# Performance work log

Hardware: AMD Instinct MI355X
Metric: run time of the kernel (lower is better)

Reference implementation:

```python
import jax, jax.numpy as jnp
import numpy as np

N = 256      # N' = N (pair rep crop size)
CZ = 128     # c_z
H = 4        # num_heads
DH = 32      # c_hidden per head
INF = 1e9
EPS = 1e-5

def setup_inputs() -> dict:
    key = jax.random.key(0)
    ks = jax.random.split(key, 8)
    s = 0.02
    return {
        "x": jax.random.normal(ks[0], (N, N, CZ), jnp.float32),
        "mask": jnp.ones((N, N), jnp.float32),
        "ln_g": jnp.ones((CZ,), jnp.float32),
        "ln_b": jnp.zeros((CZ,), jnp.float32),
        "w_tri": jax.random.normal(ks[1], (H, CZ), jnp.float32) * s,   # Linear(c_z -> H), no bias
        "wq": jax.random.normal(ks[2], (H * DH, CZ), jnp.float32) * s,
        "wk": jax.random.normal(ks[3], (H * DH, CZ), jnp.float32) * s,
        "wv": jax.random.normal(ks[4], (H * DH, CZ), jnp.float32) * s,
        "wg": jax.random.normal(ks[5], (H * DH, CZ), jnp.float32) * s,
        "bg": jnp.ones((H * DH,), jnp.float32),   # gating bias init = 1 (OpenFold)
        "wo": jax.random.normal(ks[6], (CZ, H * DH), jnp.float32) * s,
        "bo": jnp.zeros((CZ,), jnp.float32),
    }

def reference(x, mask, ln_g, ln_b, w_tri, wq, wk, wv, wg, bg, wo, bo):
    # starting=True -> no transpose. LayerNorm over c_z.
    mu = jnp.mean(x, axis=-1, keepdims=True)
    var = jnp.var(x, axis=-1, keepdims=True)
    xn = (x - mu) * jax.lax.rsqrt(var + EPS) * ln_g + ln_b        # [N', N, CZ]

    # mask bias: [*, N', 1, 1, N]
    mask_bias = (INF * (mask - 1.0))[..., :, None, None, :]
    # triangle bias: linear -> [N', N, H] -> permute (2,0,1) -> [H, N', N] -> [1, H, N', N]
    tri_bias = jnp.einsum('...ijc,hc->...hij', xn, w_tri)[..., None, :, :, :]

    scale = 1.0 / np.sqrt(DH).astype(np.float32)
    wq3, wk3, wv3, wg3 = (w.reshape(H, DH, CZ) for w in (wq, wk, wv, wg))
    q = jnp.einsum('...qc,hdc->...qhd', xn, wq3) * scale           # [N', N, H, DH]
    k = jnp.einsum('...kc,hdc->...khd', xn, wk3)
    v = jnp.einsum('...kc,hdc->...khd', xn, wv3)

    logits = jnp.einsum('...qhd,...khd->...hqk', q, k) + mask_bias + tri_bias  # [N', H, N, N]
    a = jax.nn.softmax(logits, axis=-1)
    o = jnp.einsum('...hqk,...khd->...qhd', a, v)                  # [N', N, H, DH]

    g = jax.nn.sigmoid(jnp.einsum('...qc,hdc->...qhd', xn, wg3) + bg.reshape(H, DH))
    o = (o * g).reshape(*o.shape[:-2], H * DH)                     # [N', N, H*DH]
    return jnp.einsum('...qe,oe->...qo', o, wo) + bo               # [N', N, CZ]
```

## Files before the change

kernel.cpp:

```cpp
#include <hip/hip_runtime.h>
#include <hip/hip_bf16.h>
#include <math.h>


#define NN 256
#define CZ 128
#define NH 4
#define DH 32
#define NPOS (NN * NN)
#define PSZ ((size_t)NPOS * CZ)
#define SCALE 0.17677669529663687f

typedef unsigned short ushort_t;
using f32x4  = __attribute__((ext_vector_type(4))) float;
using bf16x8 = __attribute__((ext_vector_type(8))) short;
using bf16x4 = __attribute__((ext_vector_type(4))) short;

__device__ __forceinline__ float sigmoidf_(float x) {
    return 1.0f / (1.0f + __expf(-x));
}
__device__ __forceinline__ ushort_t f2bf(float f) {
    unsigned u = __float_as_uint(f);
    u = (u + 0x7fffu + ((u >> 16) & 1u)) >> 16;
    return (ushort_t)u;
}
__device__ __forceinline__ float bf2f(ushort_t b) {
    return __uint_as_float(((unsigned)b) << 16);
}
__device__ __forceinline__ float trunc_bf(float f) {
    return __uint_as_float(__float_as_uint(f) & 0xffff0000u);
}
__device__ __forceinline__ bf16x4 pack_bf4(float a, float b, float c, float d) {
    union { unsigned u[2]; bf16x4 v; } r;
    r.u[0] = (__float_as_uint(b) & 0xffff0000u) | (__float_as_uint(a) >> 16);
    r.u[1] = (__float_as_uint(d) & 0xffff0000u) | (__float_as_uint(c) >> 16);
    return r.v;
}

__global__ __launch_bounds__(256)
void convert_weights(const float* __restrict__ wq, const float* __restrict__ wk,
                     const float* __restrict__ wv, const float* __restrict__ wg,
                     const float* __restrict__ wo,
                     ushort_t* __restrict__ Wc_hi, ushort_t* __restrict__ Wc_lo,
                     ushort_t* __restrict__ wo_hi, ushort_t* __restrict__ wo_lo) {
    int idx = blockIdx.x * 256 + threadIdx.x;
    float x;
    if (idx < 65536) {
        int t = idx >> 14;
        const float* src = (t == 0) ? wq : (t == 1) ? wk : (t == 2) ? wv : wg;
        x = src[idx & 16383];
        ushort_t h = f2bf(x);
        Wc_hi[idx] = h;
        Wc_lo[idx] = f2bf(x - bf2f(h));
    } else {
        int r = idx - 65536;
        x = wo[r];
        ushort_t h = f2bf(x);
        wo_hi[r] = h;
        wo_lo[r] = f2bf(x - bf2f(h));
    }
}

__global__ __launch_bounds__(256)
void ln_tri_kernel(const float* __restrict__ x,
                   const float* __restrict__ ln_g,
                   const float* __restrict__ ln_b,
                   const float* __restrict__ w_tri,
                   ushort_t* __restrict__ xn_hi,
                   ushort_t* __restrict__ xn_lo,
                   float* __restrict__ tri) {
    int wave = threadIdx.x >> 6;
    int lane = threadIdx.x & 63;
    int p = blockIdx.x * 4 + wave;
    const float* xp = x + (size_t)p * CZ + lane * 2;
    float2 v = *(const float2*)xp;

    float s = v.x + v.y;
    float sq = v.x * v.x + v.y * v.y;
    #pragma unroll
    for (int off = 1; off < 64; off <<= 1) {
        s  += __shfl_xor(s,  off);
        sq += __shfl_xor(sq, off);
    }
    float mu = s * (1.0f / 128.0f);
    float var = sq * (1.0f / 128.0f) - mu * mu;
    float rs = rsqrtf(var + 1e-5f);

    float2 gv = *(const float2*)(ln_g + lane * 2);
    float2 bv = *(const float2*)(ln_b + lane * 2);
    float xn0 = (v.x - mu) * rs * gv.x + bv.x;
    float xn1 = (v.y - mu) * rs * gv.y + bv.y;

    ushort_t h0 = f2bf(xn0), h1 = f2bf(xn1);
    ushort_t l0 = f2bf(xn0 - bf2f(h0)), l1 = f2bf(xn1 - bf2f(h1));
    ushort2 hh; hh.x = h0; hh.y = h1;
    ushort2 ll; ll.x = l0; ll.y = l1;
    *(ushort2*)(xn_hi + (size_t)p * CZ + lane * 2) = hh;
    *(ushort2*)(xn_lo + (size_t)p * CZ + lane * 2) = ll;

    float t0, t1, t2, t3;
    {
        float2 w0 = *(const float2*)(w_tri + 0 * CZ + lane * 2);
        float2 w1 = *(const float2*)(w_tri + 1 * CZ + lane * 2);
        float2 w2 = *(const float2*)(w_tri + 2 * CZ + lane * 2);
        float2 w3 = *(const float2*)(w_tri + 3 * CZ + lane * 2);
        t0 = xn0 * w0.x + xn1 * w0.y;
        t1 = xn0 * w1.x + xn1 * w1.y;
        t2 = xn0 * w2.x + xn1 * w2.y;
        t3 = xn0 * w3.x + xn1 * w3.y;
    }
    #pragma unroll
    for (int off = 1; off < 64; off <<= 1) {
        t0 += __shfl_xor(t0, off);
        t1 += __shfl_xor(t1, off);
        t2 += __shfl_xor(t2, off);
        t3 += __shfl_xor(t3, off);
    }
    if (lane == 0) {
        int i = p >> 8, j = p & 255;
        int kt = j >> 6, mt = (j >> 4) & 3, kg2 = (j >> 2) & 3, r = j & 3;
        int wv2 = i >> 6, nt = (i >> 4) & 3, lr2 = i & 15;
        size_t base = ((((size_t)(kt * 16 + mt * 4 + wv2)) * 4 + nt) * 64 +
                       kg2 * 16 + lr2) * 4 + r;
        tri[base + 0 * 65536] = t0;
        tri[base + 1 * 65536] = t1;
        tri[base + 2 * 65536] = t2;
        tri[base + 3 * 65536] = t3;
    }
}

template<int MODE>
__global__ __launch_bounds__(256, 2)
void gemm_split_kernel(const ushort_t* __restrict__ Ahi, const ushort_t* __restrict__ Alo,
                       const ushort_t* __restrict__ Bhi, const ushort_t* __restrict__ Blo,
                       float* __restrict__ out0, const float* __restrict__ bias,
                       ushort_t* __restrict__ qbo, ushort_t* __restrict__ kbo,
                       ushort_t* __restrict__ vto, float* __restrict__ gfo) {
    __shared__ ushort_t sA[2][128 * 64];
    __shared__ ushort_t sB[2][128 * 64];

    const int tid = threadIdx.x;
    const int bm = blockIdx.x;
    const int nb0 = blockIdx.y * 128;
    const int lane = tid & 63;
    const int wv_ = tid >> 6;
    const int wm = wv_ >> 1, wn = wv_ & 1;
    const int lr = lane & 15, kg = lane >> 4;

    f32x4 acc[4][4];
    #pragma unroll
    for (int a = 0; a < 4; a++)
        #pragma unroll
        for (int b = 0; b < 4; b++) acc[a][b] = (f32x4){0.f, 0.f, 0.f, 0.f};

    for (int k0 = 0; k0 < CZ; k0 += 64) {
        #pragma unroll
        for (int i = 0; i < 4; i++) {
            int idx = tid + i * 256;
            int row = idx >> 3, c = idx & 7;
            int lofs = row * 64 + ((c ^ (row & 7)) << 3);
            size_t ga = (size_t)(bm * 128 + row) * CZ + k0 + c * 8;
            size_t gb = (size_t)(nb0 + row) * CZ + k0 + c * 8;
            *(uint4*)&sA[0][lofs] = *(const uint4*)(Ahi + ga);
            *(uint4*)&sA[1][lofs] = *(const uint4*)(Alo + ga);
            *(uint4*)&sB[0][lofs] = *(const uint4*)(Bhi + gb);
            *(uint4*)&sB[1][lofs] = *(const uint4*)(Blo + gb);
        }
        __syncthreads();

        #pragma unroll
        for (int ks = 0; ks < 2; ks++) {
            bf16x8 ahi[4], alo[4];
            #pragma unroll
            for (int mt = 0; mt < 4; mt++) {
                int m = wm * 64 + mt * 16 + lr;
                int off = m * 64 + (((ks * 4 + kg) ^ (m & 7)) << 3);
                ahi[mt] = *(bf16x8*)&sA[0][off];
                alo[mt] = *(bf16x8*)&sA[1][off];
            }
            #pragma unroll
            for (int nt = 0; nt < 4; nt++) {
                int n = wn * 64 + nt * 16 + lr;
                int off = n * 64 + (((ks * 4 + kg) ^ (n & 7)) << 3);
                bf16x8 bhi = *(bf16x8*)&sB[0][off];
                bf16x8 blo = *(bf16x8*)&sB[1][off];
                #pragma unroll
                for (int mt = 0; mt < 4; mt++) {
                    acc[mt][nt] = __builtin_amdgcn_mfma_f32_16x16x32_bf16(ahi[mt], bhi, acc[mt][nt], 0, 0, 0);
                    acc[mt][nt] = __builtin_amdgcn_mfma_f32_16x16x32_bf16(alo[mt], bhi, acc[mt][nt], 0, 0, 0);
                    acc[mt][nt] = __builtin_amdgcn_mfma_f32_16x16x32_bf16(ahi[mt], blo, acc[mt][nt], 0, 0, 0);
                }
            }
        }
        __syncthreads();
    }

    #pragma unroll
    for (int mt = 0; mt < 4; mt++) {
        #pragma unroll
        for (int nt = 0; nt < 4; nt++) {
            int n = wn * 64 + nt * 16 + lr;
            #pragma unroll
            for (int r = 0; r < 4; r++) {
                int m = bm * 128 + wm * 64 + mt * 16 + kg * 4 + r;
                float val = acc[mt][nt][r];
                if (MODE == 0) {
                    int t = blockIdx.y;
                    int ii = m >> 8, j = m & 255;
                    int hh = n >> 5, d = n & 31;
                    size_t ihb = (size_t)((ii << 2) + hh) * 8192;
                    if (t == 0)      qbo[ihb + j * 32 + d] = f2bf(val * SCALE);
                    else if (t == 1) kbo[ihb + j * 32 + d] = f2bf(val);
                    else if (t == 2) vto[ihb + d * 256 + j] = f2bf(val);
                    else             gfo[ihb + j * 32 + d] = val;
                } else {
                    out0[(size_t)m * CZ + n] = val + bias[n];
                }
            }
        }
    }
}

__global__ __launch_bounds__(256, 4)
void attn_mfma_kernel(const ushort_t* __restrict__ qb,
                      const ushort_t* __restrict__ kb,
                      const ushort_t* __restrict__ vtb,
                      const float* __restrict__ gf,
                      const float* __restrict__ tri,
                      const float* __restrict__ mask,
                      const float* __restrict__ bg,
                      ushort_t* __restrict__ og_hi,
                      ushort_t* __restrict__ og_lo) {
    __shared__ ushort_t sV[32 * 264];

    const int bid = blockIdx.x;
    const int h = bid >> 8;
    const int i = bid & 255;
    const int tid = threadIdx.x;
    const int lane = tid & 63;
    const int wv_ = tid >> 6;
    const int lr = lane & 15;
    const int kg = lane >> 4;
    const int q0 = wv_ * 64;

    const size_t ih = (size_t)((i << 2) + h);
    const ushort_t* qp = qb + ih * 8192;
    const ushort_t* kp = kb + ih * 8192;
    const ushort_t* vp = vtb + ih * 8192;
    const float* mrow = mask + (i << 8);

    #pragma unroll
    for (int w = 0; w < 4; w++) {
        int idx = tid + w * 256;
        int d = idx >> 5, c = idx & 31;
        *(uint4*)&sV[d * 264 + c * 8] = *(const uint4*)(vp + d * 256 + c * 8);
    }

    bf16x8 qf[4];
    #pragma unroll
    for (int nt = 0; nt < 4; nt++)
        qf[nt] = *(const bf16x8*)(qp + (size_t)(q0 + nt * 16 + lr) * 32 + kg * 8);

    float tl[4] = {0.f, 0.f, 0.f, 0.f};
    f32x4 o[4][2];
    #pragma unroll
    for (int nt = 0; nt < 4; nt++) {
        o[nt][0] = (f32x4){0.f, 0.f, 0.f, 0.f};
        o[nt][1] = (f32x4){0.f, 0.f, 0.f, 0.f};
    }
    __syncthreads();

    for (int kt = 0; kt < 4; kt++) {
        const int kt0 = kt * 64;
        #pragma unroll
        for (int mt = 0; mt < 4; mt++) {
            bf16x8 ka = *(const bf16x8*)(kp + (size_t)(kt0 + mt * 16 + lr) * 32 + kg * 8);
            const float* trib = tri + ((size_t)h << 16) +
                                ((((size_t)(kt * 16 + mt * 4 + wv_)) * 4) * 64 +
                                 kg * 16 + lr) * 4;
            float4 trif[4];
            #pragma unroll
            for (int nt = 0; nt < 4; nt++)
                trif[nt] = *(const float4*)(trib + (size_t)nt * 256);
            float4 mq = *(const float4*)(mrow + kt0 + mt * 16 + kg * 4);
            float mb[4] = {(mq.x - 1.f) * 1e9f, (mq.y - 1.f) * 1e9f,
                           (mq.z - 1.f) * 1e9f, (mq.w - 1.f) * 1e9f};

            f32x4 st[4];
            #pragma unroll
            for (int nt = 0; nt < 4; nt++)
                st[nt] = __builtin_amdgcn_mfma_f32_16x16x32_bf16(
                    ka, qf[nt], (f32x4){0.f, 0.f, 0.f, 0.f}, 0, 0, 0);

            bf16x4 pa[4];
            #pragma unroll
            for (int nt = 0; nt < 4; nt++) {
                float p0 = trunc_bf(__expf(st[nt][0] + mb[0] + trif[nt].x));
                float p1 = trunc_bf(__expf(st[nt][1] + mb[1] + trif[nt].y));
                float p2 = trunc_bf(__expf(st[nt][2] + mb[2] + trif[nt].z));
                float p3 = trunc_bf(__expf(st[nt][3] + mb[3] + trif[nt].w));
                tl[nt] += (p0 + p1) + (p2 + p3);
                pa[nt] = pack_bf4(p0, p1, p2, p3);
            }
            #pragma unroll
            for (int dt = 0; dt < 2; dt++) {
                bf16x4 vb = *(const bf16x4*)&sV[(dt * 16 + lr) * 264 + kt0 + mt * 16 + kg * 4];
                #pragma unroll
                for (int nt = 0; nt < 4; nt++)
                    o[nt][dt] = __builtin_amdgcn_mfma_f32_16x16x16bf16_1k(pa[nt], vb, o[nt][dt], 0, 0, 0);
            }
        }
    }

    #pragma unroll
    for (int nt = 0; nt < 4; nt++) {
        float t = tl[nt];
        t += __shfl_xor(t, 16);
        t += __shfl_xor(t, 32);
        float inv = 1.0f / t;
        #pragma unroll
        for (int r = 0; r < 4; r++) {
            float iv = __shfl(inv, kg * 4 + r, 16);
            int q = q0 + nt * 16 + kg * 4 + r;
            #pragma unroll
            for (int dt = 0; dt < 2; dt++) {
                int d = dt * 16 + lr;
                float gate = sigmoidf_(gf[ih * 8192 + q * 32 + d] + bg[(h << 5) + d]);
                float val = o[nt][dt][r] * iv * gate;
                ushort_t vh = f2bf(val);
                ushort_t vl = f2bf(val - bf2f(vh));
                size_t ofs = (size_t)((i << 8) + q) * CZ + (h << 5) + d;
                og_hi[ofs] = vh;
                og_lo[ofs] = vl;
            }
        }
    }
}

extern "C" void kernel_launch(void* const* d_in, const int* in_sizes, int n_in,
                              void* d_out, int out_size, void* d_ws, size_t ws_size,
                              hipStream_t stream) {
    const float* x     = (const float*)d_in[0];
    const float* mask  = (const float*)d_in[1];
    const float* ln_g  = (const float*)d_in[2];
    const float* ln_b  = (const float*)d_in[3];
    const float* w_tri = (const float*)d_in[4];
    const float* wq    = (const float*)d_in[5];
    const float* wk    = (const float*)d_in[6];
    const float* wv    = (const float*)d_in[7];
    const float* wg    = (const float*)d_in[8];
    const float* bg    = (const float*)d_in[9];
    const float* wo    = (const float*)d_in[10];
    const float* bo    = (const float*)d_in[11];
    float* out = (float*)d_out;

    float* ws = (float*)d_ws;
    float* tri = ws;
    float* gf  = ws + 262144;
    ushort_t* og_hi = (ushort_t*)(gf + PSZ);
    ushort_t* og_lo = og_hi + PSZ;
    ushort_t* qbuf  = og_lo + PSZ;
    ushort_t* kbuf  = qbuf + PSZ;
    ushort_t* vtbuf = kbuf + PSZ;
    ushort_t* Wc_hi = vtbuf + PSZ;
    ushort_t* Wc_lo = Wc_hi + 65536;
    ushort_t* wo_hi = Wc_lo + 65536;
    ushort_t* wo_lo = wo_hi + 16384;
    ushort_t* xn_hi = (ushort_t*)d_out;
    ushort_t* xn_lo = xn_hi + PSZ;

    convert_weights<<<320, 256, 0, stream>>>(wq, wk, wv, wg, wo, Wc_hi, Wc_lo, wo_hi, wo_lo);
    ln_tri_kernel<<<NPOS / 4, 256, 0, stream>>>(x, ln_g, ln_b, w_tri, xn_hi, xn_lo, tri);
    gemm_split_kernel<0><<<dim3(NPOS / 128, 4), 256, 0, stream>>>(
        xn_hi, xn_lo, Wc_hi, Wc_lo, nullptr, nullptr, qbuf, kbuf, vtbuf, gf);
    attn_mfma_kernel<<<NN * NH, 256, 0, stream>>>(
        qbuf, kbuf, vtbuf, gf, tri, mask, bg, og_hi, og_lo);
    gemm_split_kernel<1><<<dim3(NPOS / 128, 1), 256, 0, stream>>>(
        og_hi, og_lo, wo_hi, wo_lo, out, bo, nullptr, nullptr, nullptr, nullptr);
}
```

Before: 259.2 us.

## Load GEMM operands directly into registers and vectorize epilogue stores

Replaces the LDS-staged split-bf16 GEMM with a kernel that loads MFMA operand fragments straight from global memory into registers. This removes the shared-memory round trip and the barriers. The MFMA operands are swapped (W as A) for the q/k/g and output paths so each lane holds four contiguous output columns, which allows 4-wide packed bf16 or float4 stores instead of scalar scattered stores. The V-transpose path keeps the original orientation so it can write 4 contiguous j values. The trade-off is that each wave now does redundant global/L2 loads, since tiles are no longer shared across waves through LDS.

```diff
diff --git a/kernel.cpp b/kernel.cpp
--- a/kernel.cpp
+++ b/kernel.cpp
@@ -34,6 +34,11 @@
     union { unsigned u[2]; bf16x4 v; } r;
     r.u[0] = (__float_as_uint(b) & 0xffff0000u) | (__float_as_uint(a) >> 16);
     r.u[1] = (__float_as_uint(d) & 0xffff0000u) | (__float_as_uint(c) >> 16);
+    return r.v;
+}
+__device__ __forceinline__ bf16x4 pack_bf4_rne(float a, float b, float c, float d) {
+    union { ushort_t s[4]; bf16x4 v; } r;
+    r.s[0] = f2bf(a); r.s[1] = f2bf(b); r.s[2] = f2bf(c); r.s[3] = f2bf(d);
     return r.v;
 }
 
@@ -130,91 +135,117 @@
 }
 
 template<int MODE>
-__global__ __launch_bounds__(256, 2)
-void gemm_split_kernel(const ushort_t* __restrict__ Ahi, const ushort_t* __restrict__ Alo,
-                       const ushort_t* __restrict__ Bhi, const ushort_t* __restrict__ Blo,
-                       float* __restrict__ out0, const float* __restrict__ bias,
-                       ushort_t* __restrict__ qbo, ushort_t* __restrict__ kbo,
-                       ushort_t* __restrict__ vto, float* __restrict__ gfo) {
-    __shared__ ushort_t sA[2][128 * 64];
-    __shared__ ushort_t sB[2][128 * 64];
-
+__global__ __launch_bounds__(256)
+void gemm_direct_kernel(const ushort_t* __restrict__ Xhi, const ushort_t* __restrict__ Xlo,
+                        const ushort_t* __restrict__ Whi, const ushort_t* __restrict__ Wlo,
+                        float* __restrict__ out0, const float* __restrict__ bias,
+                        ushort_t* __restrict__ qbo, ushort_t* __restrict__ kbo,
+                        ushort_t* __restrict__ vto, float* __restrict__ gfo) {
     const int tid = threadIdx.x;
     const int bm = blockIdx.x;
-    const int nb0 = blockIdx.y * 128;
+    const int t = (MODE == 0) ? blockIdx.y : 0;
     const int lane = tid & 63;
     const int wv_ = tid >> 6;
     const int wm = wv_ >> 1, wn = wv_ & 1;
     const int lr = lane & 15, kg = lane >> 4;
 
+    const ushort_t* xh_base = Xhi + ((size_t)(bm * 128 + wm * 64 + lr)) * CZ + kg * 8;
+    const ushort_t* xl_base = Xlo + ((size_t)(bm * 128 + wm * 64 + lr)) * CZ + kg * 8;
+    const ushort_t* wh_base = Whi + ((size_t)(t * 128 + wn * 64 + lr)) * CZ + kg * 8;
+    const ushort_t* wl_base = Wlo + ((size_t)(t * 128 + wn * 64 + lr)) * CZ + kg * 8;
+
     f32x4 acc[4][4];
     #pragma unroll
     for (int a = 0; a < 4; a++)
         #pragma unroll
         for (int b = 0; b < 4; b++) acc[a][b] = (f32x4){0.f, 0.f, 0.f, 0.f};
 
-    for (int k0 = 0; k0 < CZ; k0 += 64) {
-        #pragma unroll
-        for (int i = 0; i < 4; i++) {
-            int idx = tid + i * 256;
-            int row = idx >> 3, c = idx & 7;
-            int lofs = row * 64 + ((c ^ (row & 7)) << 3);
-            size_t ga = (size_t)(bm * 128 + row) * CZ + k0 + c * 8;
-            size_t gb = (size_t)(nb0 + row) * CZ + k0 + c * 8;
-            *(uint4*)&sA[0][lofs] = *(const uint4*)(Ahi + ga);
-            *(uint4*)&sA[1][lofs] = *(const uint4*)(Alo + ga);
-            *(uint4*)&sB[0][lofs] = *(const uint4*)(Bhi + gb);
-            *(uint4*)&sB[1][lofs] = *(const uint4*)(Blo + gb);
-        }
-        __syncthreads();
-
-        #pragma unroll
-        for (int ks = 0; ks < 2; ks++) {
-            bf16x8 ahi[4], alo[4];
-            #pragma unroll
-            for (int mt = 0; mt < 4; mt++) {
-                int m = wm * 64 + mt * 16 + lr;
-                int off = m * 64 + (((ks * 4 + kg) ^ (m & 7)) << 3);
-                ahi[mt] = *(bf16x8*)&sA[0][off];
-                alo[mt] = *(bf16x8*)&sA[1][off];
-            }
+    #pragma unroll
+    for (int ks = 0; ks < 4; ks++) {
+        bf16x8 xh[4], xl[4], wh[4], wl[4];
+        #pragma unroll
+        for (int mt = 0; mt < 4; mt++) {
+            xh[mt] = *(const bf16x8*)(xh_base + (size_t)mt * 16 * CZ + ks * 32);
+            xl[mt] = *(const bf16x8*)(xl_base + (size_t)mt * 16 * CZ + ks * 32);
+        }
+        #pragma unroll
+        for (int nt = 0; nt < 4; nt++) {
+            wh[nt] = *(const bf16x8*)(wh_base + (size_t)nt * 16 * CZ + ks * 32);
+            wl[nt] = *(const bf16x8*)(wl_base + (size_t)nt * 16 * CZ + ks * 32);
+        }
+        if (MODE == 0 && t == 2) {
+            #pragma unroll
+            for (int mt = 0; mt < 4; mt++)
+                #pragma unroll
+                for (int nt = 0; nt < 4; nt++) {
+                    acc[mt][nt] = __builtin_amdgcn_mfma_f32_16x16x32_bf16(xh[mt], wh[nt], acc[mt][nt], 0, 0, 0);
+                    acc[mt][nt] = __builtin_amdgcn_mfma_f32_16x16x32_bf16(xl[mt], wh[nt], acc[mt][nt], 0, 0, 0);
+                    acc[mt][nt] = __builtin_amdgcn_mfma_f32_16x16x32_bf16(xh[mt], wl[nt], acc[mt][nt], 0, 0, 0);
+                }
+        } else {
+            #pragma unroll
+            for (int nt = 0; nt < 4; nt++)
+                #pragma unroll
+                for (int mt = 0; mt < 4; mt++) {
+                    acc[nt][mt] = __builtin_amdgcn_mfma_f32_16x16x32_bf16(wh[nt], xh[mt], acc[nt][mt], 0, 0, 0);
+                    acc[nt][mt] = __builtin_amdgcn_mfma_f32_16x16x32_bf16(wl[nt], xh[mt], acc[nt][mt], 0, 0, 0);
+                    acc[nt][mt] = __builtin_amdgcn_mfma_f32_16x16x32_bf16(wh[nt], xl[mt], acc[nt][mt], 0, 0, 0);
+                }
+        }
+    }
+
+    if (MODE == 1) {
+        #pragma unroll
+        for (int mt = 0; mt < 4; mt++) {
+            int m = bm * 128 + wm * 64 + mt * 16 + lr;
+            #pragma unroll
+            for (int nt = 0; nt < 4; nt++) {
+                int nb = wn * 64 + nt * 16 + kg * 4;
+                float4 bv = *(const float4*)(bias + nb);
+                float4 o;
+                o.x = acc[nt][mt][0] + bv.x;
+                o.y = acc[nt][mt][1] + bv.y;
+                o.z = acc[nt][mt][2] + bv.z;
+                o.w = acc[nt][mt][3] + bv.w;
+                *(float4*)(out0 + (size_t)m * CZ + nb) = o;
+            }
+        }
+    } else if (t == 2) {
+        #pragma unroll
+        for (int mt = 0; mt < 4; mt++) {
+            int m = bm * 128 + wm * 64 + mt * 16 + kg * 4;
+            int i_ = m >> 8, jb = m & 255;
             #pragma unroll
             for (int nt = 0; nt < 4; nt++) {
                 int n = wn * 64 + nt * 16 + lr;
-                int off = n * 64 + (((ks * 4 + kg) ^ (n & 7)) << 3);
-                bf16x8 bhi = *(bf16x8*)&sB[0][off];
-                bf16x8 blo = *(bf16x8*)&sB[1][off];
-                #pragma unroll
-                for (int mt = 0; mt < 4; mt++) {
-                    acc[mt][nt] = __builtin_amdgcn_mfma_f32_16x16x32_bf16(ahi[mt], bhi, acc[mt][nt], 0, 0, 0);
-                    acc[mt][nt] = __builtin_amdgcn_mfma_f32_16x16x32_bf16(alo[mt], bhi, acc[mt][nt], 0, 0, 0);
-                    acc[mt][nt] = __builtin_amdgcn_mfma_f32_16x16x32_bf16(ahi[mt], blo, acc[mt][nt], 0, 0, 0);
-                }
-            }
-        }
-        __syncthreads();
-    }
-
-    #pragma unroll
-    for (int mt = 0; mt < 4; mt++) {
-        #pragma unroll
-        for (int nt = 0; nt < 4; nt++) {
-            int n = wn * 64 + nt * 16 + lr;
-            #pragma unroll
-            for (int r = 0; r < 4; r++) {
-                int m = bm * 128 + wm * 64 + mt * 16 + kg * 4 + r;
-                float val = acc[mt][nt][r];
-                if (MODE == 0) {
-                    int t = blockIdx.y;
-                    int ii = m >> 8, j = m & 255;
-                    int hh = n >> 5, d = n & 31;
-                    size_t ihb = (size_t)((ii << 2) + hh) * 8192;
-                    if (t == 0)      qbo[ihb + j * 32 + d] = f2bf(val * SCALE);
-                    else if (t == 1) kbo[ihb + j * 32 + d] = f2bf(val);
-                    else if (t == 2) vto[ihb + d * 256 + j] = f2bf(val);
-                    else             gfo[ihb + j * 32 + d] = val;
+                int h_ = n >> 5, d = n & 31;
+                size_t ihb = (size_t)((i_ << 2) + h_) * 8192;
+                *(bf16x4*)(vto + ihb + (size_t)d * 256 + jb) =
+                    pack_bf4_rne(acc[mt][nt][0], acc[mt][nt][1], acc[mt][nt][2], acc[mt][nt][3]);
+            }
+        }
+    } else {
+        #pragma unroll
+        for (int mt = 0; mt < 4; mt++) {
+            int m = bm * 128 + wm * 64 + mt * 16 + lr;
+            int i_ = m >> 8, jj = m & 255;
+            #pragma unroll
+            for (int nt = 0; nt < 4; nt++) {
+                int n = wn * 64 + nt * 16 + kg * 4;
+                int h_ = n >> 5, db = n & 31;
+                size_t base = (size_t)((i_ << 2) + h_) * 8192 + (size_t)jj * 32 + db;
+                if (t == 0) {
+                    *(bf16x4*)(qbo + base) = pack_bf4_rne(
+                        acc[nt][mt][0] * SCALE, acc[nt][mt][1] * SCALE,
+                        acc[nt][mt][2] * SCALE, acc[nt][mt][3] * SCALE);
+                } else if (t == 1) {
+                    *(bf16x4*)(kbo + base) = pack_bf4_rne(
+                        acc[nt][mt][0], acc[nt][mt][1], acc[nt][mt][2], acc[nt][mt][3]);
                 } else {
-                    out0[(size_t)m * CZ + n] = val + bias[n];
+                    float4 o;
+                    o.x = acc[nt][mt][0]; o.y = acc[nt][mt][1];
+                    o.z = acc[nt][mt][2]; o.w = acc[nt][mt][3];
+                    *(float4*)(gfo + base) = o;
                 }
             }
         }
@@ -371,10 +402,10 @@
 
     convert_weights<<<320, 256, 0, stream>>>(wq, wk, wv, wg, wo, Wc_hi, Wc_lo, wo_hi, wo_lo);
     ln_tri_kernel<<<NPOS / 4, 256, 0, stream>>>(x, ln_g, ln_b, w_tri, xn_hi, xn_lo, tri);
-    gemm_split_kernel<0><<<dim3(NPOS / 128, 4), 256, 0, stream>>>(
+    gemm_direct_kernel<0><<<dim3(NPOS / 128, 4), 256, 0, stream>>>(
         xn_hi, xn_lo, Wc_hi, Wc_lo, nullptr, nullptr, qbuf, kbuf, vtbuf, gf);
     attn_mfma_kernel<<<NN * NH, 256, 0, stream>>>(
         qbuf, kbuf, vtbuf, gf, tri, mask, bg, og_hi, og_lo);
-    gemm_split_kernel<1><<<dim3(NPOS / 128, 1), 256, 0, stream>>>(
+    gemm_direct_kernel<1><<<dim3(NPOS / 128, 1), 256, 0, stream>>>(
         og_hi, og_lo, wo_hi, wo_lo, out, bo, nullptr, nullptr, nullptr, nullptr);
 }
```

Result: slower. 275.5 us (+6.3%).
